# Kernel tuning notes

Hardware: AMD Instinct MI355X
Metric: run time of the kernel (lower is better)

The kernel has to match this reference:

```python
import jax, jax.numpy as jnp
import numpy as np

H = 16          # num heads
DH = 64         # head size
D = H * DH      # hidden size 1024
B, S = 2, 2048


def setup_inputs() -> dict:
    key = jax.random.key(0)
    ks = jax.random.split(key, 9)
    scale = 1.0 / np.sqrt(D)
    p = {}
    p["hidden_states"] = jax.random.normal(ks[0], (B, S, D), dtype=jnp.float32)
    for i, name in enumerate(["q", "k", "v", "o"]):
        # stored so that y = x @ W + b (transpose of torch Linear weight)
        p[f"W{name}"] = jax.random.normal(ks[1 + 2 * i], (D, D), dtype=jnp.float32) * scale
        p[f"b{name}"] = jax.random.normal(ks[2 + 2 * i], (D,), dtype=jnp.float32) * 0.01
    return p


def reference(hidden_states, Wq, bq, Wk, bk, Wv, bv, Wo, bo):
    b, s, _ = hidden_states.shape
    q = hidden_states @ Wq + bq  # [B,S,D]
    k = hidden_states @ Wk + bk
    v = hidden_states @ Wv + bv
    # [B,H,S,DH]
    q = q.reshape(b, s, H, DH).transpose(0, 2, 1, 3)
    k = k.reshape(b, s, H, DH).transpose(0, 2, 1, 3)
    v = v.reshape(b, s, H, DH).transpose(0, 2, 1, 3)
    scores = jnp.einsum("bhqd,bhkd->bhqk", q, k) / np.sqrt(DH)
    causal = jnp.triu(jnp.ones((s, s), dtype=bool), k=1)  # True above diagonal -> masked
    scores = jnp.where(causal, -jnp.inf, scores)
    attn = jax.nn.softmax(scores, axis=-1)  # dropout p=0 (eval)
    ctx = jnp.einsum("bhqk,bhkd->bhqd", attn, v)
    ctx = ctx.transpose(0, 2, 1, 3).reshape(b, s, D)
    return ctx @ Wo + bo
```

## Files before the change

### kernel.cpp

```cpp
#include <hip/hip_runtime.h>


typedef _Float16 f16x8 __attribute__((ext_vector_type(8)));
typedef _Float16 f16x4 __attribute__((ext_vector_type(4)));
typedef __fp16 h16x2 __attribute__((ext_vector_type(2)));
typedef float f32x4 __attribute__((ext_vector_type(4)));
typedef float f32x16 __attribute__((ext_vector_type(16)));

#define GLD_LDS16(g, l)                                                        \
  __builtin_amdgcn_global_load_lds(                                            \
      (__attribute__((address_space(1))) const unsigned int*)(g),              \
      (__attribute__((address_space(3))) unsigned int*)(l), 16, 0, 0)

static constexpr int Sdim = 2048;
static constexpr int Ddim = 1024;
static constexpr int NH = 16;
static constexpr int DH = 64;
static constexpr int Mrows = 4096;

static constexpr float QSCALE = 0.125f * 1.44269504f;

struct PrepArgs {
  const float* X;
  _Float16* Y;
  const float *s0, *s1, *s2, *s3;
  _Float16 *d0, *d1, *d2, *d3;
};

__global__ __launch_bounds__(256) void prep(PrepArgs a) {
  __shared__ _Float16 L[64 * 72];
  const int id = blockIdx.x, t = threadIdx.x;
  if (id >= 1024) {
    size_t i = ((size_t)(id - 1024) * 256 + t) * 8;
    float4 f0 = *(const float4*)(a.X + i);
    float4 f1 = *(const float4*)(a.X + i + 4);
    alignas(16) _Float16 h[8] = {(_Float16)f0.x, (_Float16)f0.y, (_Float16)f0.z,
                                 (_Float16)f0.w, (_Float16)f1.x, (_Float16)f1.y,
                                 (_Float16)f1.z, (_Float16)f1.w};
    *(uint4*)(a.Y + i) = *(const uint4*)h;
    return;
  }
  const int z = id >> 8;
  const float* src = z == 0 ? a.s0 : z == 1 ? a.s1 : z == 2 ? a.s2 : a.s3;
  _Float16* dst = z == 0 ? a.d0 : z == 1 ? a.d1 : z == 2 ? a.d2 : a.d3;
  const int k0 = (id & 15) * 64, n0 = ((id >> 4) & 15) * 64;
#pragma unroll
  for (int i = 0; i < 4; ++i) {
    int c = i * 256 + t;
    int row = c >> 4, cc = c & 15;
    float4 f = *(const float4*)&src[(size_t)(k0 + row) * Ddim + n0 + cc * 4];
    L[(cc * 4 + 0) * 72 + row] = (_Float16)f.x;
    L[(cc * 4 + 1) * 72 + row] = (_Float16)f.y;
    L[(cc * 4 + 2) * 72 + row] = (_Float16)f.z;
    L[(cc * 4 + 3) * 72 + row] = (_Float16)f.w;
  }
  __syncthreads();
#pragma unroll
  for (int i = 0; i < 2; ++i) {
    int c = i * 256 + t;
    int n = c >> 3, cc = c & 7;
    *(uint4*)&dst[(size_t)(n0 + n) * Ddim + k0 + cc * 8] =
        *(const uint4*)&L[n * 72 + cc * 8];
  }
}

struct GemmArgs {
  const _Float16* A;
  const _Float16 *Bt0, *Bt1, *Bt2;
  const float *b0, *b1, *b2;
  void *o0, *o1, *o2;
};

template <int MODE, int BN>
__global__ __launch_bounds__(256) void gemmT(GemmArgs g) {
  constexpr int K = 1024;
  constexpr int WN = BN / 2;
  constexpr int NI = WN / 16;
  __shared__ _Float16 As[128 * 32];
  __shared__ _Float16 Bs[BN * 32];
  const int z = blockIdx.z;
  const _Float16* A = g.A;
  const _Float16* Bt = z == 0 ? g.Bt0 : z == 1 ? g.Bt1 : g.Bt2;
  const float* bias = z == 0 ? g.b0 : z == 1 ? g.b1 : g.b2;
  void* out = z == 0 ? g.o0 : z == 1 ? g.o1 : g.o2;
  const int m0 = blockIdx.x * 128, n0 = blockIdx.y * BN;
  const int t = threadIdx.x, lane = t & 63, wv = t >> 6;
  const int wm = wv >> 1, wn = wv & 1, quad = lane >> 4, r = lane & 15;

  const int c0 = wv * 64 + lane, c1 = c0 + 256;
  const _Float16* ga0 = A + (size_t)(m0 + (c0 >> 2)) * K + (c0 & 3) * 8;
  const _Float16* ga1 = A + (size_t)(m0 + (c1 >> 2)) * K + (c1 & 3) * 8;
  const _Float16* gb0 = Bt + (size_t)(n0 + (c0 >> 2)) * K + (c0 & 3) * 8;
  const _Float16* gb1 =
      Bt + (size_t)(n0 + ((c1 >> 2) & (BN - 1))) * K + (c1 & 3) * 8;
  char* lA0 = (char*)As + (wv * 64) * 16;
  char* lA1 = (char*)As + (256 + wv * 64) * 16;
  char* lB0 = (char*)Bs + (wv * 64) * 16;
  char* lB1 = (char*)Bs + (256 + wv * 64) * 16;

  f32x4 acc[4][NI] = {};
  for (int kt = 0; kt < K; kt += 32) {
    GLD_LDS16(ga0 + kt, lA0);
    GLD_LDS16(ga1 + kt, lA1);
    GLD_LDS16(gb0 + kt, lB0);
    if constexpr (BN == 128) GLD_LDS16(gb1 + kt, lB1);
    __syncthreads();
    f16x8 af[4], bf[NI];
#pragma unroll
    for (int mi = 0; mi < 4; ++mi)
      af[mi] = *(const f16x8*)&As[(wm * 64 + mi * 16 + r) * 32 + quad * 8];
#pragma unroll
    for (int ni = 0; ni < NI; ++ni)
      bf[ni] = *(const f16x8*)&Bs[(wn * WN + ni * 16 + r) * 32 + quad * 8];
#pragma unroll
    for (int mi = 0; mi < 4; ++mi)
#pragma unroll
      for (int ni = 0; ni < NI; ++ni)
        acc[mi][ni] = __builtin_amdgcn_mfma_f32_16x16x32_f16(af[mi], bf[ni],
                                                             acc[mi][ni], 0, 0, 0);
    __syncthreads();
  }

  const float scale = (MODE == 0 && z == 0) ? QSCALE : 1.0f;
  float bv[NI];
#pragma unroll
  for (int ni = 0; ni < NI; ++ni) bv[ni] = bias[n0 + wn * WN + ni * 16 + r];
#pragma unroll
  for (int mi = 0; mi < 4; ++mi) {
#pragma unroll
    for (int ni = 0; ni < NI; ++ni) {
      const int n = n0 + wn * WN + ni * 16 + r;
      if (MODE == 0 && z == 2) {
        alignas(8) _Float16 h4[4];
#pragma unroll
        for (int reg = 0; reg < 4; ++reg)
          h4[reg] = (_Float16)(acc[mi][ni][reg] + bv[ni]);
        const int m = m0 + wm * 64 + mi * 16 + quad * 4;
        const int b = m >> 11, s = m & 2047, h = n >> 6, dh = n & 63;
        *(uint2*)&((_Float16*)out)[((size_t)(b * NH + h) * DH + dh) * Sdim + s] =
            *(const uint2*)h4;
      } else {
#pragma unroll
        for (int reg = 0; reg < 4; ++reg) {
          const int m = m0 + wm * 64 + mi * 16 + quad * 4 + reg;
          const float v = (acc[mi][ni][reg] + bv[ni]) * scale;
          if (MODE == 0) {
            const int b = m >> 11, s = m & 2047, h = n >> 6, dh = n & 63;
            ((_Float16*)out)[(((size_t)(b * NH + h) * Sdim + s) << 6) + dh] =
                (_Float16)v;
          } else {
            ((float*)out)[(size_t)m * Ddim + n] = v;
          }
        }
      }
    }
  }
}

__global__ __launch_bounds__(256) void attn(const _Float16* __restrict__ Q,
                                            const _Float16* __restrict__ Kk,
                                            const _Float16* __restrict__ Vt,
                                            _Float16* __restrict__ ctx) {
  __shared__ _Float16 Ks[2][64 * 64], Vs[2][64 * 64];
  const int id = blockIdx.x, xcd = id & 7, slot = id >> 3;
  const int qt = 31 - (slot >> 2);
  const int bh = ((slot & 3) << 3) | xcd;
  const int q0 = qt * 64;
  const int t = threadIdx.x, lane = t & 63, wv = t >> 6;
  const int qh = wv & 1, kvh = wv >> 1;
  const int n31 = lane & 31, h5 = lane >> 5, h8 = h5 * 8;
  const int b = bh >> 4, h = bh & 15;
  const _Float16* Kg = Kk + (size_t)bh * Sdim * DH;
  const _Float16* Vg = Vt + (size_t)bh * DH * Sdim;

  const int qg = q0 + qh * 32 + n31;
  const _Float16* Qrow = Q + ((size_t)bh * Sdim + qg) * DH;
  f16x8 aq[4];
#pragma unroll
  for (int ks = 0; ks < 4; ++ks) aq[ks] = *(const f16x8*)(Qrow + ks * 16 + h8);

  const int ntiles = qt + 1;
  const int sr = t >> 3, sr2 = sr + 32, sc = (t & 7) * 8;
  const int kr = (sr & 51) | ((sr & 4) << 1) | ((sr & 8) >> 1);
  const int kr2 = (sr2 & 51) | ((sr2 & 4) << 1) | ((sr2 & 8) >> 1);
  const int kc = sc ^ ((kr & 7) << 3), kc2 = sc ^ ((kr2 & 7) << 3);
  const int vc = sc ^ ((sr & 7) << 3), vc2 = sc ^ ((sr2 & 7) << 3);

  f32x16 oacc0 = {}, oacc1 = {};
  float l_i = 0.f;
  const h16x2 one2 = {(__fp16)1.0f, (__fp16)1.0f};

  uint4 ka = *(const uint4*)&Kg[(size_t)sr * DH + sc];
  uint4 kb = *(const uint4*)&Kg[(size_t)sr2 * DH + sc];
  uint4 va = *(const uint4*)&Vg[(size_t)sr * Sdim + sc];
  uint4 vb = *(const uint4*)&Vg[(size_t)sr2 * Sdim + sc];
  *(uint4*)&Ks[0][kr * 64 + kc] = ka;
  *(uint4*)&Ks[0][kr2 * 64 + kc2] = kb;
  *(uint4*)&Vs[0][sr * 64 + vc] = va;
  *(uint4*)&Vs[0][sr2 * 64 + vc2] = vb;

  const int prow = kvh * 32 + n31;
  const int pb = prow * 64, psw = (prow & 7) << 3;
  const int vsw = (n31 & 7) << 3;

  for (int it = 0; it < ntiles; ++it) {
    const int cur = it & 1;
    if (it + 1 < ntiles) {
      const int kvn = (it + 1) * 64;
      ka = *(const uint4*)&Kg[(size_t)(kvn + sr) * DH + sc];
      kb = *(const uint4*)&Kg[(size_t)(kvn + sr2) * DH + sc];
      va = *(const uint4*)&Vg[(size_t)sr * Sdim + kvn + sc];
      vb = *(const uint4*)&Vg[(size_t)sr2 * Sdim + kvn + sc];
    }
    __syncthreads();

    f32x16 sacc = {};
    __builtin_amdgcn_s_setprio(1);
#pragma unroll
    for (int ks = 0; ks < 4; ++ks) {
      f16x8 ak = *(const f16x8*)&Ks[cur][pb + ((ks * 16 + h8) ^ psw)];
      sacc = __builtin_amdgcn_mfma_f32_32x32x16_f16(ak, aq[ks], sacc, 0, 0, 0);
    }
    __builtin_amdgcn_s_setprio(0);

    const int kvb = it * 64;
    if (it == ntiles - 1) {
#pragma unroll
      for (int i = 0; i < 16; ++i) {
        const int kvgl = kvb + kvh * 32 + (i & 7) + h8 + 16 * (i >> 3);
        if (kvgl > qg) sacc[i] = -1e30f;
      }
    }
    union U { f16x8 v8; h16x2 v2[4]; } u0, u1;
#pragma unroll
    for (int i = 0; i < 4; ++i) {
      const float p0 = __builtin_amdgcn_exp2f(sacc[2 * i]);
      const float p1 = __builtin_amdgcn_exp2f(sacc[2 * i + 1]);
      u0.v2[i] = __builtin_amdgcn_cvt_pkrtz(p0, p1);
      l_i = __builtin_amdgcn_fdot2(u0.v2[i], one2, l_i, false);
    }
#pragma unroll
    for (int i = 0; i < 4; ++i) {
      const float p0 = __builtin_amdgcn_exp2f(sacc[8 + 2 * i]);
      const float p1 = __builtin_amdgcn_exp2f(sacc[9 + 2 * i]);
      u1.v2[i] = __builtin_amdgcn_cvt_pkrtz(p0, p1);
      l_i = __builtin_amdgcn_fdot2(u1.v2[i], one2, l_i, false);
    }

    __builtin_amdgcn_s_setprio(1);
#pragma unroll
    for (int ks = 0; ks < 2; ++ks) {
      const f16x8 ap = ks ? u1.v8 : u0.v8;
      const int col = kvh * 32 + ks * 16 + h8;
      f16x8 bv0 = *(const f16x8*)&Vs[cur][n31 * 64 + (col ^ vsw)];
      f16x8 bv1 = *(const f16x8*)&Vs[cur][(32 + n31) * 64 + (col ^ vsw)];
      oacc0 = __builtin_amdgcn_mfma_f32_32x32x16_f16(ap, bv0, oacc0, 0, 0, 0);
      oacc1 = __builtin_amdgcn_mfma_f32_32x32x16_f16(ap, bv1, oacc1, 0, 0, 0);
    }
    __builtin_amdgcn_s_setprio(0);

    if (it + 1 < ntiles) {
      const int nxt = cur ^ 1;
      *(uint4*)&Ks[nxt][kr * 64 + kc] = ka;
      *(uint4*)&Ks[nxt][kr2 * 64 + kc2] = kb;
      *(uint4*)&Vs[nxt][sr * 64 + vc] = va;
      *(uint4*)&Vs[nxt][sr2 * 64 + vc2] = vb;
    }
  }

  l_i += __shfl_xor(l_i, 32, 64);
  __syncthreads();
  float* obuf = (float*)&Ks[0][0] + qh * (64 * 32);
  float* lbuf = (float*)&Vs[0][0] + qh * 64;
  union V16 { f32x16 v; f32x4 q[4]; };
  if (kvh == 1) {
    V16 a, c;
    a.v = oacc0;
    c.v = oacc1;
#pragma unroll
    for (int k = 0; k < 4; ++k) {
      *(f32x4*)&obuf[lane * 32 + ((k ^ (lane & 7)) << 2)] = a.q[k];
      *(f32x4*)&obuf[lane * 32 + (((k + 4) ^ (lane & 7)) << 2)] = c.q[k];
    }
    lbuf[lane] = l_i;
  }
  __syncthreads();
  if (kvh == 0) {
    V16 a, c;
#pragma unroll
    for (int k = 0; k < 4; ++k) {
      a.q[k] = *(const f32x4*)&obuf[lane * 32 + ((k ^ (lane & 7)) << 2)];
      c.q[k] = *(const f32x4*)&obuf[lane * 32 + (((k + 4) ^ (lane & 7)) << 2)];
    }
    oacc0 += a.v;
    oacc1 += c.v;
    l_i += lbuf[lane];
#pragma unroll
    for (int rr = 0; rr < 16; ++rr) {
      const int qrow = (rr & 3) + 8 * (rr >> 2) + 4 * h5;
      const float rl = 1.0f / __shfl(l_i, qrow, 64);
      const int s = q0 + qh * 32 + qrow;
      const size_t base = ((size_t)b * Sdim + s) * Ddim + h * DH;
      ctx[base + n31] = (_Float16)(oacc0[rr] * rl);
      ctx[base + 32 + n31] = (_Float16)(oacc1[rr] * rl);
    }
  }
}

extern "C" void kernel_launch(void* const* d_in, const int* in_sizes, int n_in,
                              void* d_out, int out_size, void* d_ws,
                              size_t ws_size, hipStream_t stream) {
  const float* hid = (const float*)d_in[0];
  const float* Wq = (const float*)d_in[1];
  const float* bq = (const float*)d_in[2];
  const float* Wk = (const float*)d_in[3];
  const float* bk = (const float*)d_in[4];
  const float* Wv = (const float*)d_in[5];
  const float* bv = (const float*)d_in[6];
  const float* Wo = (const float*)d_in[7];
  const float* bo = (const float*)d_in[8];

  char* ws = (char*)d_ws;
  _Float16* Xh = (_Float16*)(ws);
  _Float16* Wqt = (_Float16*)(ws + (8ull << 20));
  _Float16* Wkt = (_Float16*)(ws + (10ull << 20));
  _Float16* Wvt = (_Float16*)(ws + (12ull << 20));
  _Float16* Wot = (_Float16*)(ws + (14ull << 20));
  _Float16* Qb = (_Float16*)(ws + (16ull << 20));
  _Float16* Kb = (_Float16*)(ws + (24ull << 20));
  _Float16* Vtb = (_Float16*)(ws + (32ull << 20));
  _Float16* ctx = Xh;

  PrepArgs pa{hid, Xh, Wq, Wk, Wv, Wo, Wqt, Wkt, Wvt, Wot};
  prep<<<dim3(3072), 256, 0, stream>>>(pa);

  GemmArgs g1{Xh, Wqt, Wkt, Wvt, bq, bk, bv, Qb, Kb, Vtb};
  gemmT<0, 128><<<dim3(Mrows / 128, Ddim / 128, 3), 256, 0, stream>>>(g1);

  attn<<<dim3(1024), 256, 0, stream>>>(Qb, Kb, Vtb, ctx);

  GemmArgs g2{ctx, Wot, Wot, Wot, bo, bo, bo, d_out, d_out, d_out};
  gemmT<1, 64><<<dim3(Mrows / 128, Ddim / 64, 1), 256, 0, stream>>>(g2);
}
```

Before: 175.5 us.

## Switch projection GEMMs to 32x32x16 MFMA with BK=64 k-tiles

Rewrites the QKV and output projection GEMM inner loop to use 32x32x16 MFMA instructions instead of 16x16x32, and doubles the K tile from 32 to 64. The aim is fewer LDS fragment reads per MFMA, half as many barrier pairs per K loop, and better operand reuse. The epilogue is remapped to the 32x32 accumulator layout. LDS use doubles, the row-major 128-byte stride may cause bank conflicts, and a larger accumulator could raise register pressure.

Measured after the change: 204.5 us. 16.5% more time.

```diff
diff --git a/kernel.cpp b/kernel.cpp
--- a/kernel.cpp
+++ b/kernel.cpp
@@ -74,10 +74,12 @@
 template <int MODE, int BN>
 __global__ __launch_bounds__(256) void gemmT(GemmArgs g) {
   constexpr int K = 1024;
+  constexpr int BK = 64;
   constexpr int WN = BN / 2;
-  constexpr int NI = WN / 16;
-  __shared__ _Float16 As[128 * 32];
-  __shared__ _Float16 Bs[BN * 32];
+  constexpr int NI = WN / 32;
+  constexpr int BCH = BN * 8;
+  __shared__ _Float16 As[128 * BK];
+  __shared__ _Float16 Bs[BN * BK];
   const int z = blockIdx.z;
   const _Float16* A = g.A;
   const _Float16* Bt = z == 0 ? g.Bt0 : z == 1 ? g.Bt1 : g.Bt2;
@@ -85,65 +87,79 @@
   void* out = z == 0 ? g.o0 : z == 1 ? g.o1 : g.o2;
   const int m0 = blockIdx.x * 128, n0 = blockIdx.y * BN;
   const int t = threadIdx.x, lane = t & 63, wv = t >> 6;
-  const int wm = wv >> 1, wn = wv & 1, quad = lane >> 4, r = lane & 15;
-
-  const int c0 = wv * 64 + lane, c1 = c0 + 256;
-  const _Float16* ga0 = A + (size_t)(m0 + (c0 >> 2)) * K + (c0 & 3) * 8;
-  const _Float16* ga1 = A + (size_t)(m0 + (c1 >> 2)) * K + (c1 & 3) * 8;
-  const _Float16* gb0 = Bt + (size_t)(n0 + (c0 >> 2)) * K + (c0 & 3) * 8;
-  const _Float16* gb1 =
-      Bt + (size_t)(n0 + ((c1 >> 2) & (BN - 1))) * K + (c1 & 3) * 8;
-  char* lA0 = (char*)As + (wv * 64) * 16;
-  char* lA1 = (char*)As + (256 + wv * 64) * 16;
-  char* lB0 = (char*)Bs + (wv * 64) * 16;
-  char* lB1 = (char*)Bs + (256 + wv * 64) * 16;
-
-  f32x4 acc[4][NI] = {};
-  for (int kt = 0; kt < K; kt += 32) {
-    GLD_LDS16(ga0 + kt, lA0);
-    GLD_LDS16(ga1 + kt, lA1);
-    GLD_LDS16(gb0 + kt, lB0);
-    if constexpr (BN == 128) GLD_LDS16(gb1 + kt, lB1);
+  const int wm = wv >> 1, wn = wv & 1;
+  const int n31 = lane & 31, h5 = lane >> 5, h8 = h5 * 8;
+
+  const _Float16* ga[4];
+  const _Float16* gb[4];
+  char* lA[4];
+  char* lB[4];
+#pragma unroll
+  for (int i = 0; i < 4; ++i) {
+    const int c = i * 256 + t;
+    ga[i] = A + (size_t)(m0 + (c >> 3)) * K + (c & 7) * 8;
+    lA[i] = (char*)As + (i * 256 + wv * 64) * 16;
+  }
+#pragma unroll
+  for (int i = 0; i < BCH / 256; ++i) {
+    const int c = i * 256 + t;
+    gb[i] = Bt + (size_t)(n0 + (c >> 3)) * K + (c & 7) * 8;
+    lB[i] = (char*)Bs + (i * 256 + wv * 64) * 16;
+  }
+
+  f32x16 acc[2][NI] = {};
+  for (int kt = 0; kt < K; kt += BK) {
+#pragma unroll
+    for (int i = 0; i < 4; ++i) GLD_LDS16(ga[i] + kt, lA[i]);
+#pragma unroll
+    for (int i = 0; i < BCH / 256; ++i) GLD_LDS16(gb[i] + kt, lB[i]);
     __syncthreads();
-    f16x8 af[4], bf[NI];
-#pragma unroll
-    for (int mi = 0; mi < 4; ++mi)
-      af[mi] = *(const f16x8*)&As[(wm * 64 + mi * 16 + r) * 32 + quad * 8];
-#pragma unroll
-    for (int ni = 0; ni < NI; ++ni)
-      bf[ni] = *(const f16x8*)&Bs[(wn * WN + ni * 16 + r) * 32 + quad * 8];
-#pragma unroll
-    for (int mi = 0; mi < 4; ++mi)
-#pragma unroll
-      for (int ni = 0; ni < NI; ++ni)
-        acc[mi][ni] = __builtin_amdgcn_mfma_f32_16x16x32_f16(af[mi], bf[ni],
-                                                             acc[mi][ni], 0, 0, 0);
+#pragma unroll
+    for (int ks = 0; ks < 4; ++ks) {
+      const int kc = ks * 16 + h8;
+      f16x8 a0 = *(const f16x8*)&As[(wm * 64 + n31) * BK + kc];
+      f16x8 a1 = *(const f16x8*)&As[(wm * 64 + 32 + n31) * BK + kc];
+#pragma unroll
+      for (int ni = 0; ni < NI; ++ni) {
+        f16x8 bf = *(const f16x8*)&Bs[(wn * WN + ni * 32 + n31) * BK + kc];
+        acc[0][ni] =
+            __builtin_amdgcn_mfma_f32_32x32x16_f16(a0, bf, acc[0][ni], 0, 0, 0);
+        acc[1][ni] =
+            __builtin_amdgcn_mfma_f32_32x32x16_f16(a1, bf, acc[1][ni], 0, 0, 0);
+      }
+    }
     __syncthreads();
   }
 
   const float scale = (MODE == 0 && z == 0) ? QSCALE : 1.0f;
   float bv[NI];
 #pragma unroll
-  for (int ni = 0; ni < NI; ++ni) bv[ni] = bias[n0 + wn * WN + ni * 16 + r];
-#pragma unroll
-  for (int mi = 0; mi < 4; ++mi) {
+  for (int ni = 0; ni < NI; ++ni) bv[ni] = bias[n0 + wn * WN + ni * 32 + n31];
+#pragma unroll
+  for (int mi = 0; mi < 2; ++mi) {
 #pragma unroll
     for (int ni = 0; ni < NI; ++ni) {
-      const int n = n0 + wn * WN + ni * 16 + r;
+      const int n = n0 + wn * WN + ni * 32 + n31;
       if (MODE == 0 && z == 2) {
-        alignas(8) _Float16 h4[4];
-#pragma unroll
-        for (int reg = 0; reg < 4; ++reg)
-          h4[reg] = (_Float16)(acc[mi][ni][reg] + bv[ni]);
-        const int m = m0 + wm * 64 + mi * 16 + quad * 4;
-        const int b = m >> 11, s = m & 2047, h = n >> 6, dh = n & 63;
-        *(uint2*)&((_Float16*)out)[((size_t)(b * NH + h) * DH + dh) * Sdim + s] =
-            *(const uint2*)h4;
+        const int b = (m0 >> 11), h = n >> 6, dh = n & 63;
+#pragma unroll
+        for (int hi = 0; hi < 4; ++hi) {
+          alignas(8) _Float16 h4[4];
+#pragma unroll
+          for (int j = 0; j < 4; ++j)
+            h4[j] = (_Float16)(acc[mi][ni][hi * 4 + j] + bv[ni]);
+          const int m = m0 + wm * 64 + mi * 32 + 8 * hi + 4 * h5;
+          const int s = m & 2047;
+          *(uint2*)&(
+              (_Float16*)out)[((size_t)(b * NH + h) * DH + dh) * Sdim + s] =
+              *(const uint2*)h4;
+        }
       } else {
 #pragma unroll
-        for (int reg = 0; reg < 4; ++reg) {
-          const int m = m0 + wm * 64 + mi * 16 + quad * 4 + reg;
-          const float v = (acc[mi][ni][reg] + bv[ni]) * scale;
+        for (int rr = 0; rr < 16; ++rr) {
+          const int m =
+              m0 + wm * 64 + mi * 32 + (rr & 3) + 8 * (rr >> 2) + 4 * h5;
+          const float v = (acc[mi][ni][rr] + bv[ni]) * scale;
           if (MODE == 0) {
             const int b = m >> 11, s = m & 2047, h = n >> 6, dh = n & 63;
             ((_Float16*)out)[(((size_t)(b * NH + h) * Sdim + s) << 6) + dh] =
```
